# Performance work log

Measured on AMD Instinct MI355X. Metric: run time of the kernel, lower is better.

## Reference

```python
import jax, jax.numpy as jnp
import numpy as np

N, C, D = 64, 4, 2048
K = 64          # kernel_size (shapelet length)
O = 256         # out_channels (number of shapelets)
L = D - K + 1   # number of sliding windows


def setup_inputs() -> dict:
    key = jax.random.key(0)
    k1, k2 = jax.random.split(key)
    x_input = jax.random.normal(k1, (N, C, D), dtype=jnp.float32)
    weight = jax.random.normal(k2, (O, C, K), dtype=jnp.float32)
    return {"x_input": x_input, "weight": weight}


def reference(x_input, weight):
    # im2col: sliding windows of length K -> (n, c, L, K)
    idx = jnp.arange(L)[:, None] + jnp.arange(K)[None, :]  # (L, K)
    windows = x_input[:, :, idx]                            # (n, c, L, K)
    # pairwise squared distances per channel, normalized by K
    x_norm = jnp.sum(windows * windows, axis=-1)            # (n, c, L)
    y_norm = jnp.sum(weight * weight, axis=-1)              # (o, c)
    cross = jnp.einsum('nclk,ock->ncol', windows, weight)   # (n, c, o, L)
    dist = (x_norm[:, :, None, :] + y_norm.T[None, :, :, None] - 2.0 * cross)
    dist = jnp.maximum(dist, 0.0) / K                       # clamp(., 0, inf) / len
    return dist  # (n, in_channels, out_channels, L)
```

## Files before the change

### kernel.cpp

```cpp
#include <hip/hip_runtime.h>

#define N_ 64
#define C_ 4
#define D_ 2048
#define K_ 64
#define O_ 256
#define L_ 1985
#define XCOPY 2116
#define SPITCH 2012
#define NTILE 125

typedef __attribute__((ext_vector_type(8))) short s16x8;
typedef __attribute__((ext_vector_type(4))) float f32x4;

#define BAR_LGKM() do { \
    asm volatile("s_waitcnt lgkmcnt(0)\n\ts_barrier" ::: "memory"); \
    __builtin_amdgcn_sched_barrier(0); \
} while (0)

__device__ __forceinline__ unsigned short f2bf(float f) {
    union { float f; unsigned u; } v; v.f = f;
    unsigned u = v.u;
    u += 0x7fffu + ((u >> 16) & 1u);
    return (unsigned short)(u >> 16);
}

__device__ __forceinline__ float bf2f(unsigned short b) {
    union { unsigned u; float f; } v;
    v.u = (unsigned)b << 16;
    return v.f;
}

__global__ __launch_bounds__(256) void prep_w(const float* __restrict__ w,
                                              unsigned short* __restrict__ wb,
                                              float* __restrict__ ynK) {
    int o = blockIdx.x;
    int tid = threadIdx.x;
    int c = tid >> 6, k = tid & 63;
    size_t idx = (size_t)(o * C_ + c) * K_ + k;
    float v = w[idx];
    wb[idx] = f2bf(v);
    float s = v * v;
    for (int off = 32; off > 0; off >>= 1) s += __shfl_down(s, off, 64);
    if (k == 0) ynK[o * C_ + c] = s * 0.015625f;
}

__global__ __launch_bounds__(1024) void shapelet_main(const float* __restrict__ x,
                                                      const unsigned short* __restrict__ wb,
                                                      const float* __restrict__ ynK,
                                                      float* __restrict__ out) {
    __shared__ __align__(16) unsigned short xs[4][XCOPY];
    __shared__ float xn[D_];
    __shared__ __align__(16) unsigned short stg[2][16 * SPITCH];

    int nc = blockIdx.x;
    int c = nc & (C_ - 1);
    const float* xrow = x + (size_t)nc * D_;
    int tid = threadIdx.x;

    float* z    = (float*)stg;
    float* pre  = (float*)stg + 2176;
    float* S16v = (float*)stg + 4288;

    for (int i = tid; i < 2112; i += 1024) {
        float v = (i < D_) ? xrow[i] : 0.f;
        z[i] = v * v;
        unsigned short b = f2bf(v);
        #pragma unroll
        for (int s = 0; s < 4; ++s) { int j = i - s; if (j >= 0) xs[s][j] = b; }
    }
    __syncthreads();
    if (tid < 132) {
        float run = 0.f;
        int base = tid * 16;
        #pragma unroll
        for (int j = 0; j < 16; ++j) { pre[base + j] = run; run += z[base + j]; }
        S16v[tid] = run;
    }
    __syncthreads();
    for (int l = tid; l < D_; l += 1024) {
        int a = l >> 4, b = l & 15;
        float s = S16v[a] - pre[a * 16 + b] + S16v[a + 1] + S16v[a + 2]
                + S16v[a + 3] + pre[(a + 4) * 16 + b];
        xn[l] = s * 0.015625f;
    }
    __syncthreads();

    int wave = tid >> 6, lane = tid & 63, lr = lane & 15, hi = lane >> 4;
    const unsigned short* xbase = &xs[lr & 3][(lr & ~3) + hi * 8];
    int dj = lane;

    auto compute_band = [&](int st, int p) {
        int o = st * 16 + lr;
        const s16x8* wp = reinterpret_cast<const s16x8*>(
            wb + ((size_t)o * C_ + c) * K_ + hi * 8);
        s16x8 w0 = wp[0];
        s16x8 w1 = wp[4];
        float ynKv = ynK[o * C_ + c];
        #pragma unroll
        for (int i = 0; i < 8; ++i) {
            int t = wave + i * 16;
            int tc = t > 124 ? 124 : t;
            int l0t = tc * 16;
            union { unsigned long long u[2]; s16x8 v; } a0, a1;
            const unsigned long long* p0 = (const unsigned long long*)(xbase + l0t);
            a0.u[0] = p0[0]; a0.u[1] = p0[1];
            const unsigned long long* p1 = (const unsigned long long*)(xbase + l0t + 32);
            a1.u[0] = p1[0]; a1.u[1] = p1[1];
            f32x4 acc = {0.f, 0.f, 0.f, 0.f};
            acc = __builtin_amdgcn_mfma_f32_16x16x32_bf16(a0.v, w0, acc, 0, 0, 0);
            acc = __builtin_amdgcn_mfma_f32_16x16x32_bf16(a1.v, w1, acc, 0, 0, 0);
            f32x4 xv = *reinterpret_cast<const f32x4*>(&xn[l0t + hi * 4]);
            float r0 = fmaxf(fmaf(acc[0], -0.03125f, xv[0] + ynKv), 0.f);
            float r1 = fmaxf(fmaf(acc[1], -0.03125f, xv[1] + ynKv), 0.f);
            float r2 = fmaxf(fmaf(acc[2], -0.03125f, xv[2] + ynKv), 0.f);
            float r3 = fmaxf(fmaf(acc[3], -0.03125f, xv[3] + ynKv), 0.f);
            unsigned long long pk =
                  (unsigned long long)f2bf(r0)
                | ((unsigned long long)f2bf(r1) << 16)
                | ((unsigned long long)f2bf(r2) << 32)
                | ((unsigned long long)f2bf(r3) << 48);
            if (t < NTILE)
                *(unsigned long long*)&stg[p][lr * SPITCH + l0t + hi * 4] = pk;
        }
    };

    auto drain_band = [&](int b, int pb) {
        float* gb = out + ((size_t)nc * O_ + b * 16 + wave) * L_;
        const unsigned short* src = &stg[pb][wave * SPITCH];
        #pragma unroll
        for (int q = 0; q < 8; ++q) {
            int pos = dj * 4 + q * 256;
            if (pos + 4 <= L_) {
                unsigned long long dv = *(const unsigned long long*)(src + pos);
                f32x4 v;
                v[0] = bf2f((unsigned short)(dv));
                v[1] = bf2f((unsigned short)(dv >> 16));
                v[2] = bf2f((unsigned short)(dv >> 32));
                v[3] = bf2f((unsigned short)(dv >> 48));
                __builtin_memcpy(gb + pos, &v, 16);
            }
        }
        if (dj == 0) gb[L_ - 1] = bf2f(src[L_ - 1]);
    };

    bool drain_first = (wave & 1);
    for (int st = 0; st < 16; ++st) {
        int p = st & 1;
        if (drain_first && st > 0) drain_band(st - 1, p ^ 1);
        compute_band(st, p);
        if (!drain_first && st > 0) drain_band(st - 1, p ^ 1);
        BAR_LGKM();
    }
    drain_band(15, 1);
}

extern "C" void kernel_launch(void* const* d_in, const int* in_sizes, int n_in,
                              void* d_out, int out_size, void* d_ws, size_t ws_size,
                              hipStream_t stream) {
    const float* x = (const float*)d_in[0];
    const float* w = (const float*)d_in[1];
    float* out = (float*)d_out;

    unsigned short* wb = (unsigned short*)d_ws;
    float* ynK = (float*)((char*)d_ws + (size_t)O_ * C_ * K_ * 2);

    prep_w<<<O_, 256, 0, stream>>>(w, wb, ynK);
    shapelet_main<<<N_ * C_, 1024, 0, stream>>>(x, wb, ynK, out);
}
```

Measured before the change: 119.0 us.

## Use eight shifted bf16 input copies and vectorized 16-byte LDS drain

Replaces the four shifted bf16 copies of the input row with eight copies whose rows are 16-byte aligned. Each MFMA operand then loads with a single 128-bit LDS read instead of two 64-bit reads. The x-norm values are read into registers once before the band loop, which drops the separate xn shared array and its per-tile LDS reads. The staging pitch changes so that rows are 16-byte aligned, letting the drain read eight bf16 values per LDS access and issue two 16-byte global stores per lane. The alternating drain-first order across waves is dropped. The cost is more LDS work and space at setup for the extra copies and the temporary float row.

```diff
diff --git a/kernel.cpp b/kernel.cpp
--- a/kernel.cpp
+++ b/kernel.cpp
@@ -6,8 +6,8 @@
 #define K_ 64
 #define O_ 256
 #define L_ 1985
-#define XCOPY 2116
-#define SPITCH 2012
+#define XSW 2056
+#define SPITCH 2008
 #define NTILE 125
 
 typedef __attribute__((ext_vector_type(8))) short s16x8;
@@ -24,11 +24,11 @@
     u += 0x7fffu + ((u >> 16) & 1u);
     return (unsigned short)(u >> 16);
 }
-
-__device__ __forceinline__ float bf2f(unsigned short b) {
-    union { unsigned u; float f; } v;
-    v.u = (unsigned)b << 16;
-    return v.f;
+__device__ __forceinline__ float bflo(unsigned u) {
+    union { unsigned x; float f; } v; v.x = u << 16; return v.f;
+}
+__device__ __forceinline__ float bfhi(unsigned u) {
+    union { unsigned x; float f; } v; v.x = u & 0xffff0000u; return v.f;
 }
 
 __global__ __launch_bounds__(256) void prep_w(const float* __restrict__ w,
@@ -49,8 +49,7 @@
                                                       const unsigned short* __restrict__ wb,
                                                       const float* __restrict__ ynK,
                                                       float* __restrict__ out) {
-    __shared__ __align__(16) unsigned short xs[4][XCOPY];
-    __shared__ float xn[D_];
+    __shared__ __align__(16) unsigned short xs8[8][XSW];
     __shared__ __align__(16) unsigned short stg[2][16 * SPITCH];
 
     int nc = blockIdx.x;
@@ -58,18 +57,22 @@
     const float* xrow = x + (size_t)nc * D_;
     int tid = threadIdx.x;
 
-    float* z    = (float*)stg;
-    float* pre  = (float*)stg + 2176;
-    float* S16v = (float*)stg + 4288;
+    float* xf   = (float*)stg;
+    float* z    = (float*)stg + 2112;
+    float* pre  = (float*)stg + 4288;
+    float* S16v = (float*)stg + 6400;
+    float* xnl  = (float*)stg + 6592;
 
     for (int i = tid; i < 2112; i += 1024) {
         float v = (i < D_) ? xrow[i] : 0.f;
+        xf[i] = v;
         z[i] = v * v;
-        unsigned short b = f2bf(v);
-        #pragma unroll
-        for (int s = 0; s < 4; ++s) { int j = i - s; if (j >= 0) xs[s][j] = b; }
     }
     __syncthreads();
+    for (int j = tid; j < XSW; j += 1024) {
+        #pragma unroll
+        for (int s = 0; s < 8; ++s) xs8[s][j] = f2bf(xf[j + s]);
+    }
     if (tid < 132) {
         float run = 0.f;
         int base = tid * 16;
@@ -78,39 +81,72 @@
         S16v[tid] = run;
     }
     __syncthreads();
-    for (int l = tid; l < D_; l += 1024) {
+    for (int l = tid; l < 2000; l += 1024) {
         int a = l >> 4, b = l & 15;
         float s = S16v[a] - pre[a * 16 + b] + S16v[a + 1] + S16v[a + 2]
                 + S16v[a + 3] + pre[(a + 4) * 16 + b];
-        xn[l] = s * 0.015625f;
+        xnl[l] = s * 0.015625f;
     }
     __syncthreads();
 
     int wave = tid >> 6, lane = tid & 63, lr = lane & 15, hi = lane >> 4;
-    const unsigned short* xbase = &xs[lr & 3][(lr & ~3) + hi * 8];
+    const unsigned short* xsc = xs8[lr & 7];
     int dj = lane;
 
-    auto compute_band = [&](int st, int p) {
+    f32x4 xnr[8];
+    #pragma unroll
+    for (int i = 0; i < 8; ++i) {
+        int t = wave + i * 16;
+        int tc = t > 124 ? 124 : t;
+        xnr[i] = *reinterpret_cast<const f32x4*>(&xnl[tc * 16 + hi * 4]);
+    }
+    __syncthreads();
+
+    auto drain_band = [&](int b, int pb) {
+        float* gb = out + ((size_t)nc * O_ + b * 16 + wave) * L_;
+        const unsigned short* src = &stg[pb][wave * SPITCH];
+        #pragma unroll
+        for (int q = 0; q < 4; ++q) {
+            int pos = dj * 8 + q * 512;
+            if (pos + 8 <= L_) {
+                s16x8 dv = *reinterpret_cast<const s16x8*>(src + pos);
+                const unsigned* du = (const unsigned*)&dv;
+                f32x4 v0, v1;
+                v0[0] = bflo(du[0]); v0[1] = bfhi(du[0]);
+                v0[2] = bflo(du[1]); v0[3] = bfhi(du[1]);
+                v1[0] = bflo(du[2]); v1[1] = bfhi(du[2]);
+                v1[2] = bflo(du[3]); v1[3] = bfhi(du[3]);
+                __builtin_memcpy(gb + pos, &v0, 16);
+                __builtin_memcpy(gb + pos + 4, &v1, 16);
+            }
+        }
+        if (dj == 0) {
+            union { unsigned x; float f; } v; v.x = (unsigned)src[L_ - 1] << 16;
+            gb[L_ - 1] = v.f;
+        }
+    };
+
+    for (int st = 0; st < 16; ++st) {
+        int p = st & 1;
         int o = st * 16 + lr;
         const s16x8* wp = reinterpret_cast<const s16x8*>(
             wb + ((size_t)o * C_ + c) * K_ + hi * 8);
         s16x8 w0 = wp[0];
         s16x8 w1 = wp[4];
         float ynKv = ynK[o * C_ + c];
+
         #pragma unroll
         for (int i = 0; i < 8; ++i) {
             int t = wave + i * 16;
             int tc = t > 124 ? 124 : t;
             int l0t = tc * 16;
-            union { unsigned long long u[2]; s16x8 v; } a0, a1;
-            const unsigned long long* p0 = (const unsigned long long*)(xbase + l0t);
-            a0.u[0] = p0[0]; a0.u[1] = p0[1];
-            const unsigned long long* p1 = (const unsigned long long*)(xbase + l0t + 32);
-            a1.u[0] = p1[0]; a1.u[1] = p1[1];
+            int ja = l0t + (lr & ~7) + hi * 8;
+            s16x8 a0 = *reinterpret_cast<const s16x8*>(&xsc[ja]);
+            s16x8 a1 = *reinterpret_cast<const s16x8*>(&xsc[ja + 32]);
             f32x4 acc = {0.f, 0.f, 0.f, 0.f};
-            acc = __builtin_amdgcn_mfma_f32_16x16x32_bf16(a0.v, w0, acc, 0, 0, 0);
-            acc = __builtin_amdgcn_mfma_f32_16x16x32_bf16(a1.v, w1, acc, 0, 0, 0);
-            f32x4 xv = *reinterpret_cast<const f32x4*>(&xn[l0t + hi * 4]);
+            acc = __builtin_amdgcn_mfma_f32_16x16x32_bf16(a0, w0, acc, 0, 0, 0);
+            acc = __builtin_amdgcn_mfma_f32_16x16x32_bf16(a1, w1, acc, 0, 0, 0);
+            f32x4 xv = xnr[i];
             float r0 = fmaxf(fmaf(acc[0], -0.03125f, xv[0] + ynKv), 0.f);
             float r1 = fmaxf(fmaf(acc[1], -0.03125f, xv[1] + ynKv), 0.f);
             float r2 = fmaxf(fmaf(acc[2], -0.03125f, xv[2] + ynKv), 0.f);
@@ -123,33 +159,8 @@
             if (t < NTILE)
                 *(unsigned long long*)&stg[p][lr * SPITCH + l0t + hi * 4] = pk;
         }
-    };
 
-    auto drain_band = [&](int b, int pb) {
-        float* gb = out + ((size_t)nc * O_ + b * 16 + wave) * L_;
-        const unsigned short* src = &stg[pb][wave * SPITCH];
-        #pragma unroll
-        for (int q = 0; q < 8; ++q) {
-            int pos = dj * 4 + q * 256;
-            if (pos + 4 <= L_) {
-                unsigned long long dv = *(const unsigned long long*)(src + pos);
-                f32x4 v;
-                v[0] = bf2f((unsigned short)(dv));
-                v[1] = bf2f((unsigned short)(dv >> 16));
-                v[2] = bf2f((unsigned short)(dv >> 32));
-                v[3] = bf2f((unsigned short)(dv >> 48));
-                __builtin_memcpy(gb + pos, &v, 16);
-            }
-        }
-        if (dj == 0) gb[L_ - 1] = bf2f(src[L_ - 1]);
-    };
-
-    bool drain_first = (wave & 1);
-    for (int st = 0; st < 16; ++st) {
-        int p = st & 1;
-        if (drain_first && st > 0) drain_band(st - 1, p ^ 1);
-        compute_band(st, p);
-        if (!drain_first && st > 0) drain_band(st - 1, p ^ 1);
+        if (st > 0) drain_band(st - 1, p ^ 1);
         BAR_LGKM();
     }
     drain_band(15, 1);
```

After: 116.0 us. 2.5% less time.
